# Optimization experiments

Hardware: AMD Instinct MI355X
Metric: run time of the kernel (lower is better)

Reference implementation:

```python
import jax, jax.numpy as jnp
import numpy as np

N = 80000      # num nodes total (8 graphs x 10000 vars)
E = 2560000    # num edges (avg degree 32)
EMB = 64       # embedding_layer_dim
POS = 16       # positional_features_dims
DG = 64        # dim_gnn
IN0 = 2 * EMB + POS          # 144, first conv in
IN1 = DG + 2 * EMB           # 192, second conv in / BN dim
EPS = 1e-5


def _lin_init(key, fan_in, fan_out):
    return jax.random.normal(key, (fan_in, fan_out), jnp.float32) / np.sqrt(fan_in)


def setup_inputs() -> dict:
    key = jax.random.key(0)
    ks = jax.random.split(key, 16)
    inp = {}
    inp["x1"] = jax.random.normal(ks[0], (N, EMB), jnp.float32)
    inp["x2"] = jax.random.normal(ks[1], (N, EMB), jnp.float32)
    inp["random_dims"] = jax.random.normal(ks[2], (N, POS), jnp.float32)
    inp["batch"] = jnp.sort(jax.random.randint(ks[3], (N,), 0, 8)).astype(jnp.int64)
    inp["x_j_mask"] = jnp.ones((E,), jnp.float32)
    inp["edge_index"] = jax.random.randint(ks[4], (2, E), 0, N).astype(jnp.int64)
    # GCNConv weights (PyG: lin then aggregate, bias added after)
    inp["conv0_w"] = _lin_init(ks[5], IN0, DG)
    inp["conv0_b"] = jnp.zeros((DG,), jnp.float32)
    inp["conv1_w"] = _lin_init(ks[6], IN1, DG)
    inp["conv1_b"] = jnp.zeros((DG,), jnp.float32)
    # BatchNorms after each conv (dim = DG + 2*EMB = 192)
    inp["bn0_g"] = jnp.ones((IN1,), jnp.float32)
    inp["bn0_b"] = jnp.zeros((IN1,), jnp.float32)
    inp["bn1_g"] = jnp.ones((IN1,), jnp.float32)
    inp["bn1_b"] = jnp.zeros((IN1,), jnp.float32)
    # MLP head: mlp[:-2] = [192->64, 64->64], mlp[-2] = 64->32 (final ->1 not applied here)
    inp["mlp0_w"] = _lin_init(ks[7], IN1, DG)
    inp["mlp0_b"] = jnp.zeros((DG,), jnp.float32)
    inp["mlp1_w"] = _lin_init(ks[8], DG, DG)
    inp["mlp1_b"] = jnp.zeros((DG,), jnp.float32)
    inp["mlp2_w"] = _lin_init(ks[9], DG, DG // 2)
    inp["mlp2_b"] = jnp.zeros((DG // 2,), jnp.float32)
    inp["bnm0_g"] = jnp.ones((DG,), jnp.float32)
    inp["bnm0_b"] = jnp.zeros((DG,), jnp.float32)
    inp["bnm1_g"] = jnp.ones((DG,), jnp.float32)
    inp["bnm1_b"] = jnp.zeros((DG,), jnp.float32)
    inp["bnm2_g"] = jnp.ones((DG // 2,), jnp.float32)
    inp["bnm2_b"] = jnp.zeros((DG // 2,), jnp.float32)
    return inp


def _batchnorm(x, g, b):
    m = x.mean(axis=0)
    v = jnp.var(x, axis=0)  # biased var, as torch BN uses for normalization
    return (x - m) * jax.lax.rsqrt(v + EPS) * g + b


def _gcn_conv(x, w, b, row, col, coef):
    # coef = deg^-1/2[row] * deg^-1/2[col] * x_j_mask, per edge
    h = x @ w                                   # [N, out]
    msg = coef[:, None] * h[row]                # gather + scale, [E, out]
    agg = jax.ops.segment_sum(msg, col, num_segments=N)
    return agg + b


def reference(x1, x2, random_dims, batch, x_j_mask, edge_index,
              conv0_w, conv0_b, conv1_w, conv1_b,
              bn0_g, bn0_b, bn1_g, bn1_b,
              mlp0_w, mlp0_b, mlp1_w, mlp1_b, mlp2_w, mlp2_b,
              bnm0_g, bnm0_b, bnm1_g, bnm1_b, bnm2_g, bnm2_b):
    row, col = edge_index[0], edge_index[1]
    # gcn_norm with add_self_loops=False, unit edge weights
    deg = jax.ops.segment_sum(jnp.ones((E,), x1.dtype), col, num_segments=N)
    dis = jnp.where(deg > 0, jax.lax.rsqrt(jnp.maximum(deg, 1.0)), 0.0)
    coef = dis[row] * dis[col] * x_j_mask       # edge mutilation mask applied to messages

    x = jnp.concatenate([x1, x2, random_dims], axis=1)  # [N, 144]
    # GNN layer 0
    h = jax.nn.elu(_gcn_conv(x, conv0_w, conv0_b, row, col, coef))
    x = _batchnorm(jnp.concatenate([x1, x2, h], axis=1), bn0_g, bn0_b)
    # GNN layer 1
    h = jax.nn.elu(_gcn_conv(x, conv1_w, conv1_b, row, col, coef))
    x = _batchnorm(jnp.concatenate([x1, x2, h], axis=1), bn1_g, bn1_b)
    # MLP head (from_node_to_out: mlp[:-2] with bns_mlp[:-1], then mlp[-2] with bns_mlp[-1])
    x = _batchnorm(jax.nn.elu(x @ mlp0_w + mlp0_b), bnm0_g, bnm0_b)
    x = _batchnorm(jax.nn.elu(x @ mlp1_w + mlp1_b), bnm1_g, bnm1_b)
    x = _batchnorm(jax.nn.elu(x @ mlp2_w + mlp2_b), bnm2_g, bnm2_b)
    return x  # [N, DG//2]
```

## Files before the change

kernel.cpp:

```cpp
#include <hip/hip_runtime.h>
#include <hip/hip_fp16.h>
#include <math.h>

#define NN 80000
#define NE 2560000
#define NBK 313
#define BCAP 10240
#define BN_EPS 1e-5f

typedef __attribute__((ext_vector_type(8))) short short8;
typedef __attribute__((ext_vector_type(8))) unsigned short ushort8;
typedef __attribute__((ext_vector_type(4))) float f32x4;

#define OFF_DIS     0
#define OFF_ROWPTR  80000
#define OFF_CURSOR  160004
#define OFF_DEG     240004
#define OFF_PERM    320004
#define OFF_XB      (OFF_PERM + 2*NE)
#define OFF_RDB     (OFF_XB + NN*64)
#define OFF_B1      (OFF_RDB + NN*16)
#define OFF_B2      (OFF_B1 + NN*32)
#define OFF_B3      (OFF_B2 + NN*32)
#define OFF_WP      (OFF_B3 + NN*32)
#define OFF_BV      (OFF_WP + 20480)
#define OFF_STATS   (OFF_BV + 320)

__device__ __forceinline__ ushort f2b(float f) {
    union { float f; unsigned u; } x; x.f = f;
    return (ushort)((x.u + 0x7FFF + ((x.u >> 16) & 1)) >> 16);
}
__device__ __forceinline__ float b2f(ushort u) {
    union { unsigned u; float f; } x; x.u = ((unsigned)u) << 16;
    return x.f;
}
__device__ __forceinline__ float h2f(unsigned bits15) {
    __half_raw hr; hr.x = (unsigned short)(bits15 & 0x7FFFu);
    return __half2float(*(__half*)&hr);
}

__global__ void __launch_bounds__(256) k_scat1(const int* __restrict__ erow,
                                               const int* __restrict__ ecol,
                                               const float* __restrict__ mask,
                                               int* __restrict__ bcursor,
                                               int2* __restrict__ pbuf) {
    __shared__ int hist[NBK], base[NBK];
    for (int i = threadIdx.x; i < NBK; i += 256) hist[i] = 0;
    __syncthreads();
    int e0 = blockIdx.x * 4096;
    int r[16], c[16], rk[16];
    float mk[16];
    #pragma unroll
    for (int i = 0; i < 16; i++) {
        int e = e0 + i * 256 + threadIdx.x;
        if (e < NE) {
            r[i] = erow[e]; c[i] = ecol[e]; mk[i] = mask[e];
            rk[i] = atomicAdd(&hist[c[i] >> 8], 1);
        } else c[i] = -1;
    }
    __syncthreads();
    for (int b = threadIdx.x; b < NBK; b += 256) {
        int h = hist[b];
        base[b] = h ? atomicAdd(&bcursor[b], h) : 0;
    }
    __syncthreads();
    #pragma unroll
    for (int i = 0; i < 16; i++) {
        if (c[i] >= 0) {
            int b = c[i] >> 8;
            int off = base[b] + rk[i];
            if (off < BCAP)
                pbuf[b * BCAP + off] = make_int2((r[i] << 8) | (c[i] & 255), __float_as_int(mk[i]));
        }
    }
}

__global__ void __launch_bounds__(256) k_cnt(const int* __restrict__ bcursor,
                                             const int2* __restrict__ pbuf,
                                             int* __restrict__ deg) {
    __shared__ int hist[256];
    int b = blockIdx.x, c0 = b << 8;
    int ncols = (NN - c0) < 256 ? (NN - c0) : 256;
    hist[threadIdx.x] = 0;
    __syncthreads();
    int cnt = bcursor[b];
    for (int i = threadIdx.x; i < cnt; i += 256)
        atomicAdd(&hist[pbuf[b * BCAP + i].x & 255], 1);
    __syncthreads();
    if (threadIdx.x < ncols) deg[c0 + threadIdx.x] = hist[threadIdx.x];
}

__global__ void __launch_bounds__(512) k_scanB(const int* __restrict__ bcursor,
                                               int* __restrict__ boff,
                                               int* __restrict__ rowptr) {
    __shared__ int s[512];
    int t = threadIdx.x;
    int v = t < NBK ? bcursor[t] : 0;
    s[t] = v;
    __syncthreads();
    for (int off = 1; off < 512; off <<= 1) {
        int u = t >= off ? s[t - off] : 0;
        __syncthreads();
        s[t] += u;
        __syncthreads();
    }
    if (t < NBK) boff[t] = s[t] - v;
    if (t == NBK - 1) rowptr[NN] = s[t];
}

__global__ void k_dis(const int* __restrict__ deg, float* __restrict__ dis) {
    int i = blockIdx.x * blockDim.x + threadIdx.x;
    if (i < NN) {
        int d = deg[i];
        dis[i] = d > 0 ? rsqrtf((float)d) : 0.f;
    }
}

__global__ void __launch_bounds__(256) k_place(const int* __restrict__ bcursor,
                                               const int* __restrict__ boff,
                                               const int* __restrict__ deg,
                                               const float* __restrict__ dis,
                                               const int2* __restrict__ pbuf,
                                               int* __restrict__ rowptr,
                                               unsigned* __restrict__ perm) {
    __shared__ int s[256], rbase[256], lcur[256];
    __shared__ float sdis[256];
    int b = blockIdx.x, c0 = b << 8;
    int ncols = (NN - c0) < 256 ? (NN - c0) : 256;
    int t = threadIdx.x;
    int d = t < ncols ? deg[c0 + t] : 0;
    s[t] = d;
    lcur[t] = 0;
    if (t < ncols) sdis[t] = dis[c0 + t];
    __syncthreads();
    for (int off = 1; off < 256; off <<= 1) {
        int u = t >= off ? s[t - off] : 0;
        __syncthreads();
        s[t] += u;
        __syncthreads();
    }
    rbase[t] = s[t] - d;
    __syncthreads();
    int gb = boff[b];
    if (t < ncols) rowptr[c0 + t] = gb + rbase[t];
    int cnt = bcursor[b];
    for (int i = t; i < cnt; i += 256) {
        int2 rec = pbuf[b * BCAP + i];
        int crel = rec.x & 255;
        unsigned row = (unsigned)(rec.x >> 8);
        float coef = dis[row] * sdis[crel] * __int_as_float(rec.y);
        __half hh = __float2half(coef);
        unsigned hb = (unsigned)__half_as_ushort(hh) & 0x7FFFu;
        int slot = gb + rbase[crel] + atomicAdd(&lcur[crel], 1);
        perm[slot] = (row << 15) | hb;
    }
}

__global__ void __launch_bounds__(256) k_prepstats(const float* __restrict__ x1,
                                                   const float* __restrict__ x2,
                                                   const float* __restrict__ rd,
                                                   ushort* __restrict__ xb,
                                                   ushort* __restrict__ rdb,
                                                   float* __restrict__ st) {
    int wave = threadIdx.x >> 6, lane = threadIdx.x & 63;
    float s1 = 0, q1 = 0, s2 = 0, q2 = 0;
    for (int n = blockIdx.x * 4 + wave; n < NN; n += gridDim.x * 4) {
        float a = x1[(size_t)n * 64 + lane];
        float b = x2[(size_t)n * 64 + lane];
        s1 += a; q1 += a * a; s2 += b; q2 += b * b;
        xb[(size_t)n * 128 + lane]      = f2b(a);
        xb[(size_t)n * 128 + 64 + lane] = f2b(b);
        if (lane < 32)
            rdb[(size_t)n * 32 + lane] = lane < 16 ? f2b(rd[(size_t)n * 16 + lane]) : 0;
    }
    __shared__ float red[4][256];
    red[0][threadIdx.x] = s1; red[1][threadIdx.x] = q1;
    red[2][threadIdx.x] = s2; red[3][threadIdx.x] = q2;
    __syncthreads();
    if (threadIdx.x < 64) {
        int l = threadIdx.x;
        atomicAdd(&st[l],       red[0][l] + red[0][l+64] + red[0][l+128] + red[0][l+192]);
        atomicAdd(&st[128 + l], red[1][l] + red[1][l+64] + red[1][l+128] + red[1][l+192]);
        atomicAdd(&st[64 + l],  red[2][l] + red[2][l+64] + red[2][l+128] + red[2][l+192]);
        atomicAdd(&st[192 + l], red[3][l] + red[3][l+64] + red[3][l+128] + red[3][l+192]);
    }
}

__global__ void k_foldw0(const float* __restrict__ W, ushort* __restrict__ Wp) {
    for (int idx = threadIdx.x; idx < 160 * 64; idx += 256) {
        int k = idx >> 6, c = idx & 63;
        float val = k < 144 ? W[k * 64 + c] : 0.f;
        int ks = k >> 5, j = k & 7, kg = (k >> 3) & 3;
        int l = kg * 16 + (c & 15), ct = c >> 4;
        Wp[((ks * 4 + ct) * 64 + l) * 8 + j] = f2b(val);
    }
}

__global__ void k_bnfold192(const float* __restrict__ xs,
                            const float* __restrict__ hsum, const float* __restrict__ hsq,
                            const float* __restrict__ g, const float* __restrict__ bnb,
                            const float* __restrict__ W,
                            const float* __restrict__ bias,
                            ushort* __restrict__ Wp, float* __restrict__ bvec) {
    __shared__ float scale[192], shift[192];
    int t = threadIdx.x;
    if (t < 192) {
        float s = t < 128 ? xs[t] : hsum[t - 128];
        float q = t < 128 ? xs[128 + t] : hsq[t - 128];
        float m = s * (1.f / NN);
        float var = q * (1.f / NN) - m * m;
        float sc = g[t] * rsqrtf(var + BN_EPS);
        scale[t] = sc;
        shift[t] = bnb[t] - m * sc;
    }
    __syncthreads();
    for (int idx = t; idx < 192 * 64; idx += 256) {
        int k = idx >> 6, c = idx & 63;
        float val = scale[k] * W[idx];
        int ks = k >> 5, j = k & 7, kg = (k >> 3) & 3;
        int l = kg * 16 + (c & 15), ct = c >> 4;
        Wp[((ks * 4 + ct) * 64 + l) * 8 + j] = f2b(val);
    }
    if (t < 64) {
        float acc = bias ? bias[t] : 0.f;
        for (int k = 0; k < 192; k++) acc += shift[k] * W[k * 64 + t];
        bvec[t] = acc;
    }
}

__global__ void k_bnfold64(const float* __restrict__ sum, const float* __restrict__ sq,
                           const float* __restrict__ g, const float* __restrict__ bnb,
                           const float* __restrict__ W, const float* __restrict__ bias,
                           ushort* __restrict__ Wp, float* __restrict__ bvec, int NCw) {
    __shared__ float scale[64], shift[64];
    int t = threadIdx.x;
    if (t < 64) {
        float m = sum[t] * (1.f / NN);
        float var = sq[t] * (1.f / NN) - m * m;
        float sc = g[t] * rsqrtf(var + BN_EPS);
        scale[t] = sc;
        shift[t] = bnb[t] - m * sc;
    }
    __syncthreads();
    int NCOLT = NCw >> 4;
    for (int idx = t; idx < 64 * NCw; idx += 256) {
        int k = idx / NCw, c = idx % NCw;
        float val = scale[k] * W[idx];
        int ks = k >> 5, j = k & 7, kg = (k >> 3) & 3;
        int l = kg * 16 + (c & 15), ct = c >> 4;
        Wp[((ks * NCOLT + ct) * 64 + l) * 8 + j] = f2b(val);
    }
    if (t < NCw) {
        float acc = bias[t];
        for (int k = 0; k < 64; k++) acc += shift[k] * W[k * NCw + t];
        bvec[t] = acc;
    }
}

template <int KSTEPS, int NCOLT, int KS1, int S1, int S2, bool EPI, bool OUTF32>
__global__ void __launch_bounds__(256) k_mfma(const ushort* __restrict__ A1,
                                              const ushort* __restrict__ A2,
                                              const ushort* __restrict__ Wp,
                                              const float* __restrict__ bvec,
                                              void* __restrict__ out,
                                              float* __restrict__ sum,
                                              float* __restrict__ sq) {
    const int NC = NCOLT * 16;
    __shared__ float cs[NC], cq[NC];
    int wave = threadIdx.x >> 6, lane = threadIdx.x & 63;
    int r0 = lane & 15, kg = lane >> 4;
    int rbase = blockIdx.x * 64 + wave * 16;
    if (EPI) {
        if (threadIdx.x < NC) { cs[threadIdx.x] = 0.f; cq[threadIdx.x] = 0.f; }
        __syncthreads();
    }
    f32x4 acc[NCOLT];
    #pragma unroll
    for (int ct = 0; ct < NCOLT; ct++) acc[ct] = (f32x4){0.f, 0.f, 0.f, 0.f};
    #pragma unroll
    for (int ks = 0; ks < KSTEPS; ks++) {
        const ushort* src = (ks < KS1)
            ? A1 + (size_t)(rbase + r0) * S1 + ks * 32 + kg * 8
            : A2 + (size_t)(rbase + r0) * S2 + (ks - KS1) * 32 + kg * 8;
        short8 a = *reinterpret_cast<const short8*>(src);
        #pragma unroll
        for (int ct = 0; ct < NCOLT; ct++) {
            short8 b = *reinterpret_cast<const short8*>(Wp + ((size_t)(ks * NCOLT + ct) * 64 + lane) * 8);
            acc[ct] = __builtin_amdgcn_mfma_f32_16x16x32_bf16(a, b, acc[ct], 0, 0, 0);
        }
    }
    float ss[NCOLT], qq[NCOLT];
    #pragma unroll
    for (int ct = 0; ct < NCOLT; ct++) {
        int c = ct * 16 + r0;
        float bv = bvec[c];
        ss[ct] = 0.f; qq[ct] = 0.f;
        #pragma unroll
        for (int r = 0; r < 4; r++) {
            int row = rbase + kg * 4 + r;
            float v = acc[ct][r] + bv;
            if (EPI) {
                v = v > 0.f ? v : (__expf(v) - 1.f);
                ss[ct] += v; qq[ct] += v * v;
            }
            if (OUTF32) ((float*)out)[(size_t)row * NC + c] = v;
            else        ((ushort*)out)[(size_t)row * NC + c] = f2b(v);
        }
    }
    if (EPI) {
        #pragma unroll
        for (int ct = 0; ct < NCOLT; ct++) {
            int c = ct * 16 + r0;
            atomicAdd(&cs[c], ss[ct]);
            atomicAdd(&cq[c], qq[ct]);
        }
        __syncthreads();
        if (threadIdx.x < NC) {
            atomicAdd(&sum[threadIdx.x], cs[threadIdx.x]);
            atomicAdd(&sq[threadIdx.x], cq[threadIdx.x]);
        }
    }
}

__global__ void __launch_bounds__(256) k_gather(const int* __restrict__ rowptr,
                                                const unsigned* __restrict__ perm,
                                                const ushort* __restrict__ h,
                                                const float* __restrict__ bias,
                                                ushort* __restrict__ out,
                                                float* __restrict__ sum,
                                                float* __restrict__ sq) {
    __shared__ float cs[64], cq[64];
    if (threadIdx.x < 64) { cs[threadIdx.x] = 0.f; cq[threadIdx.x] = 0.f; }
    __syncthreads();
    int wave = threadIdx.x >> 6, lane = threadIdx.x & 63;
    int g = lane >> 3, c8 = lane & 7;
    const ushort* hb = h + c8 * 8;
    float bs[8];
    #pragma unroll
    for (int j = 0; j < 8; j++) bs[j] = bias[c8 * 8 + j];
    float sArr[8], qArr[8];
    #pragma unroll
    for (int j = 0; j < 8; j++) { sArr[j] = 0.f; qArr[j] = 0.f; }

    for (int n = blockIdx.x * 4 + wave; n < NN; n += gridDim.x * 4) {
        int beg = rowptr[n], end = rowptr[n + 1];
        float acc[8];
        #pragma unroll
        for (int j = 0; j < 8; j++) acc[j] = 0.f;
        int e = beg;
        for (; e + 32 <= end; e += 32) {
            unsigned p0 = perm[e + g];
            unsigned p1 = perm[e + 8 + g];
            unsigned p2 = perm[e + 16 + g];
            unsigned p3 = perm[e + 24 + g];
            ushort8 h0 = *reinterpret_cast<const ushort8*>(hb + (size_t)(p0 >> 15) * 64);
            ushort8 h1 = *reinterpret_cast<const ushort8*>(hb + (size_t)(p1 >> 15) * 64);
            ushort8 h2 = *reinterpret_cast<const ushort8*>(hb + (size_t)(p2 >> 15) * 64);
            ushort8 h3 = *reinterpret_cast<const ushort8*>(hb + (size_t)(p3 >> 15) * 64);
            float c0 = h2f(p0), c1 = h2f(p1), c2 = h2f(p2), c3 = h2f(p3);
            #pragma unroll
            for (int j = 0; j < 8; j++) {
                acc[j] += c0 * b2f(h0[j]);
                acc[j] += c1 * b2f(h1[j]);
                acc[j] += c2 * b2f(h2[j]);
                acc[j] += c3 * b2f(h3[j]);
            }
        }
        for (; e < end; e += 8) {
            int ee = e + g;
            unsigned p = ee < end ? perm[ee] : 0u;
            ushort8 hv = *reinterpret_cast<const ushort8*>(hb + (size_t)(p >> 15) * 64);
            float cf = h2f(p);
            #pragma unroll
            for (int j = 0; j < 8; j++) acc[j] += cf * b2f(hv[j]);
        }
        #pragma unroll
        for (int j = 0; j < 8; j++) {
            float a = acc[j];
            a += __shfl_xor(a, 8, 64);
            a += __shfl_xor(a, 16, 64);
            a += __shfl_xor(a, 32, 64);
            acc[j] = a;
        }
        if (g == 0) {
            ushort8 ov;
            #pragma unroll
            for (int j = 0; j < 8; j++) {
                float v = acc[j] + bs[j];
                v = v > 0.f ? v : (__expf(v) - 1.f);
                sArr[j] += v; qArr[j] += v * v;
                ov[j] = f2b(v);
            }
            *reinterpret_cast<ushort8*>(out + (size_t)n * 64 + c8 * 8) = ov;
        }
    }
    if (g == 0) {
        #pragma unroll
        for (int j = 0; j < 8; j++) {
            atomicAdd(&cs[c8 * 8 + j], sArr[j]);
            atomicAdd(&cq[c8 * 8 + j], qArr[j]);
        }
    }
    __syncthreads();
    if (threadIdx.x < 64) {
        atomicAdd(&sum[threadIdx.x], cs[threadIdx.x]);
        atomicAdd(&sq[threadIdx.x], cq[threadIdx.x]);
    }
}

__global__ void k_out(const float* __restrict__ u2, const float* __restrict__ sum,
                      const float* __restrict__ sq, const float* __restrict__ g,
                      const float* __restrict__ bb, float* __restrict__ out) {
    int t = blockIdx.x * blockDim.x + threadIdx.x;
    if (t < NN * 32) {
        int c = t & 31;
        float m = sum[c] * (1.f / NN);
        float var = sq[c] * (1.f / NN) - m * m;
        float sc = g[c] * rsqrtf(var + BN_EPS);
        float sh = bb[c] - m * sc;
        out[t] = u2[t] * sc + sh;
    }
}

extern "C" void kernel_launch(void* const* d_in, const int* in_sizes, int n_in,
                              void* d_out, int out_size, void* d_ws, size_t ws_size,
                              hipStream_t stream) {
    const float* x1 = (const float*)d_in[0];
    const float* x2 = (const float*)d_in[1];
    const float* rd = (const float*)d_in[2];
    const float* mask = (const float*)d_in[4];
    const int* ei = (const int*)d_in[5];
    const int* erow = ei;
    const int* ecol = ei + NE;
    const float* conv0_w = (const float*)d_in[6];
    const float* conv0_b = (const float*)d_in[7];
    const float* conv1_w = (const float*)d_in[8];
    const float* conv1_b = (const float*)d_in[9];
    const float* bn0_g = (const float*)d_in[10];
    const float* bn0_b = (const float*)d_in[11];
    const float* bn1_g = (const float*)d_in[12];
    const float* bn1_b = (const float*)d_in[13];
    const float* mlp0_w = (const float*)d_in[14];
    const float* mlp0_b = (const float*)d_in[15];
    const float* mlp1_w = (const float*)d_in[16];
    const float* mlp1_b = (const float*)d_in[17];
    const float* mlp2_w = (const float*)d_in[18];
    const float* mlp2_b = (const float*)d_in[19];
    const float* bnm0_g = (const float*)d_in[20];
    const float* bnm0_b = (const float*)d_in[21];
    const float* bnm1_g = (const float*)d_in[22];
    const float* bnm1_b = (const float*)d_in[23];
    const float* bnm2_g = (const float*)d_in[24];
    const float* bnm2_b = (const float*)d_in[25];

    float* ws = (float*)d_ws;
    float* dis = ws + OFF_DIS;
    int* rowptr = (int*)(ws + OFF_ROWPTR);
    int* bcursor = (int*)(ws + OFF_CURSOR);
    int* boff = bcursor + 2048;
    int* deg = (int*)(ws + OFF_DEG);
    unsigned* perm = (unsigned*)(ws + OFF_PERM);
    ushort* xb = (ushort*)(ws + OFF_XB);
    ushort* rdb = (ushort*)(ws + OFF_RDB);
    ushort* B1 = (ushort*)(ws + OFF_B1);
    ushort* B2 = (ushort*)(ws + OFF_B2);
    ushort* B3 = (ushort*)(ws + OFF_B3);
    int2* pbuf = (int2*)(ws + OFF_B1);
    ushort* wp = (ushort*)(ws + OFF_WP);
    ushort* WP0 = wp, *WP1 = wp + 10240, *WP2 = wp + 22528, *WP3 = wp + 34816, *WP4 = wp + 38912;
    float* bv = ws + OFF_BV;
    float* st = ws + OFF_STATS;

    hipMemsetAsync(bcursor, 0, (size_t)1024 * 4, stream);
    hipMemsetAsync(bv, 0, (size_t)(320 + 1920) * 4, stream);

    k_scat1<<<(NE + 4095) / 4096, 256, 0, stream>>>(erow, ecol, mask, bcursor, pbuf);
    k_cnt<<<NBK, 256, 0, stream>>>(bcursor, pbuf, deg);
    k_scanB<<<1, 512, 0, stream>>>(bcursor, boff, rowptr);
    k_dis<<<NBK, 256, 0, stream>>>(deg, dis);
    k_place<<<NBK, 256, 0, stream>>>(bcursor, boff, deg, dis, pbuf, rowptr, perm);
    k_prepstats<<<1024, 256, 0, stream>>>(x1, x2, rd, xb, rdb, st);
    k_foldw0<<<1, 256, 0, stream>>>(conv0_w, WP0);

    const int GB = NN / 64;

    k_mfma<5, 4, 4, 128, 32, false, false><<<GB, 256, 0, stream>>>(xb, rdb, WP0, bv, B1, nullptr, nullptr);
    k_gather<<<2048, 256, 0, stream>>>(rowptr, perm, B1, conv0_b, B2, st + 256, st + 320);
    k_bnfold192<<<1, 256, 0, stream>>>(st, st + 256, st + 320, bn0_g, bn0_b, conv1_w, nullptr, WP1, bv + 64);

    k_mfma<6, 4, 4, 128, 64, false, false><<<GB, 256, 0, stream>>>(xb, B2, WP1, bv + 64, B1, nullptr, nullptr);
    k_gather<<<2048, 256, 0, stream>>>(rowptr, perm, B1, conv1_b, B3, st + 384, st + 448);
    k_bnfold192<<<1, 256, 0, stream>>>(st, st + 384, st + 448, bn1_g, bn1_b, mlp0_w, mlp0_b, WP2, bv + 128);

    k_mfma<6, 4, 4, 128, 64, true, false><<<GB, 256, 0, stream>>>(xb, B3, WP2, bv + 128, B2, st + 512, st + 576);
    k_bnfold64<<<1, 256, 0, stream>>>(st + 512, st + 576, bnm0_g, bnm0_b, mlp1_w, mlp1_b, WP3, bv + 192, 64);
    k_mfma<2, 4, 2, 64, 64, true, false><<<GB, 256, 0, stream>>>(B2, nullptr, WP3, bv + 192, B1, st + 640, st + 704);
    k_bnfold64<<<1, 256, 0, stream>>>(st + 640, st + 704, bnm1_g, bnm1_b, mlp2_w, mlp2_b, WP4, bv + 256, 32);
    k_mfma<2, 2, 2, 64, 64, true, true><<<GB, 256, 0, stream>>>(B1, nullptr, WP4, bv + 256, B3, st + 768, st + 800);
    k_out<<<(NN * 32 + 255) / 256, 256, 0, stream>>>((const float*)B3, st + 768, st + 800,
                                                     bnm2_g, bnm2_b, (float*)d_out);
}
```

Baseline: 606.4 us.

## Fuse CSR build kernels and fold source-degree scaling into GEMM epilogue

Merges the degree count, rsqrt-degree and placement kernels into one per-bucket build kernel, so there are fewer launches and no round trip through global deg. The source-side dis[row] factor moves out of edge-coefficient construction and into the conv GEMM epilogues, scaling each output row once. That removes a random dis gather per edge. The edge list is widened to int2 with an fp32 coefficient instead of packed row plus fp16, which doubles the bytes each gather reads per edge. The gather's main and tail loops are merged into one predicated loop.

```diff
diff --git a/kernel.cpp b/kernel.cpp
--- a/kernel.cpp
+++ b/kernel.cpp
@@ -34,10 +34,6 @@
     union { unsigned u; float f; } x; x.u = ((unsigned)u) << 16;
     return x.f;
 }
-__device__ __forceinline__ float h2f(unsigned bits15) {
-    __half_raw hr; hr.x = (unsigned short)(bits15 & 0x7FFFu);
-    return __half2float(*(__half*)&hr);
-}
 
 __global__ void __launch_bounds__(256) k_scat1(const int* __restrict__ erow,
                                                const int* __restrict__ ecol,
@@ -75,21 +71,6 @@
     }
 }
 
-__global__ void __launch_bounds__(256) k_cnt(const int* __restrict__ bcursor,
-                                             const int2* __restrict__ pbuf,
-                                             int* __restrict__ deg) {
-    __shared__ int hist[256];
-    int b = blockIdx.x, c0 = b << 8;
-    int ncols = (NN - c0) < 256 ? (NN - c0) : 256;
-    hist[threadIdx.x] = 0;
-    __syncthreads();
-    int cnt = bcursor[b];
-    for (int i = threadIdx.x; i < cnt; i += 256)
-        atomicAdd(&hist[pbuf[b * BCAP + i].x & 255], 1);
-    __syncthreads();
-    if (threadIdx.x < ncols) deg[c0 + threadIdx.x] = hist[threadIdx.x];
-}
-
 __global__ void __launch_bounds__(512) k_scanB(const int* __restrict__ bcursor,
                                                int* __restrict__ boff,
                                                int* __restrict__ rowptr) {
@@ -108,30 +89,29 @@
     if (t == NBK - 1) rowptr[NN] = s[t];
 }
 
-__global__ void k_dis(const int* __restrict__ deg, float* __restrict__ dis) {
-    int i = blockIdx.x * blockDim.x + threadIdx.x;
-    if (i < NN) {
-        int d = deg[i];
-        dis[i] = d > 0 ? rsqrtf((float)d) : 0.f;
-    }
-}
-
-__global__ void __launch_bounds__(256) k_place(const int* __restrict__ bcursor,
+__global__ void __launch_bounds__(256) k_build(const int* __restrict__ bcursor,
                                                const int* __restrict__ boff,
-                                               const int* __restrict__ deg,
-                                               const float* __restrict__ dis,
                                                const int2* __restrict__ pbuf,
+                                               float* __restrict__ dis,
                                                int* __restrict__ rowptr,
-                                               unsigned* __restrict__ perm) {
-    __shared__ int s[256], rbase[256], lcur[256];
+                                               int2* __restrict__ perm) {
+    __shared__ int hist[256], s[256], rbase[256], lcur[256];
     __shared__ float sdis[256];
     int b = blockIdx.x, c0 = b << 8;
     int ncols = (NN - c0) < 256 ? (NN - c0) : 256;
     int t = threadIdx.x;
-    int d = t < ncols ? deg[c0 + t] : 0;
+    hist[t] = 0;
+    lcur[t] = 0;
+    __syncthreads();
+    int cnt = bcursor[b];
+    for (int i = t; i < cnt; i += 256)
+        atomicAdd(&hist[pbuf[b * BCAP + i].x & 255], 1);
+    __syncthreads();
+    int d = (t < ncols) ? hist[t] : 0;
+    float dv = d > 0 ? rsqrtf((float)d) : 0.f;
+    sdis[t] = dv;
+    if (t < ncols) dis[c0 + t] = dv;
     s[t] = d;
-    lcur[t] = 0;
-    if (t < ncols) sdis[t] = dis[c0 + t];
     __syncthreads();
     for (int off = 1; off < 256; off <<= 1) {
         int u = t >= off ? s[t - off] : 0;
@@ -143,16 +123,13 @@
     __syncthreads();
     int gb = boff[b];
     if (t < ncols) rowptr[c0 + t] = gb + rbase[t];
-    int cnt = bcursor[b];
     for (int i = t; i < cnt; i += 256) {
         int2 rec = pbuf[b * BCAP + i];
         int crel = rec.x & 255;
-        unsigned row = (unsigned)(rec.x >> 8);
-        float coef = dis[row] * sdis[crel] * __int_as_float(rec.y);
-        __half hh = __float2half(coef);
-        unsigned hb = (unsigned)__half_as_ushort(hh) & 0x7FFFu;
+        int row = rec.x >> 8;
+        float coefS = sdis[crel] * __int_as_float(rec.y);
         int slot = gb + rbase[crel] + atomicAdd(&lcur[crel], 1);
-        perm[slot] = (row << 15) | hb;
+        perm[slot] = make_int2(row, __float_as_int(coefS));
     }
 }
 
@@ -257,11 +234,12 @@
     }
 }
 
-template <int KSTEPS, int NCOLT, int KS1, int S1, int S2, bool EPI, bool OUTF32>
+template <int KSTEPS, int NCOLT, int KS1, int S1, int S2, bool EPI, bool OUTF32, int DISW>
 __global__ void __launch_bounds__(256) k_mfma(const ushort* __restrict__ A1,
                                               const ushort* __restrict__ A2,
                                               const ushort* __restrict__ Wp,
                                               const float* __restrict__ bvec,
+                                              const float* __restrict__ disw,
                                               void* __restrict__ out,
                                               float* __restrict__ sum,
                                               float* __restrict__ sq) {
@@ -289,6 +267,11 @@
             acc[ct] = __builtin_amdgcn_mfma_f32_16x16x32_bf16(a, b, acc[ct], 0, 0, 0);
         }
     }
+    float dsv[4];
+    if (DISW) {
+        #pragma unroll
+        for (int r = 0; r < 4; r++) dsv[r] = disw[rbase + kg * 4 + r];
+    }
     float ss[NCOLT], qq[NCOLT];
     #pragma unroll
     for (int ct = 0; ct < NCOLT; ct++) {
@@ -299,6 +282,7 @@
         for (int r = 0; r < 4; r++) {
             int row = rbase + kg * 4 + r;
             float v = acc[ct][r] + bv;
+            if (DISW) v *= dsv[r];
             if (EPI) {
                 v = v > 0.f ? v : (__expf(v) - 1.f);
                 ss[ct] += v; qq[ct] += v * v;
@@ -323,7 +307,7 @@
 }
 
 __global__ void __launch_bounds__(256) k_gather(const int* __restrict__ rowptr,
-                                                const unsigned* __restrict__ perm,
+                                                const int2* __restrict__ perm,
                                                 const ushort* __restrict__ h,
                                                 const float* __restrict__ bias,
                                                 ushort* __restrict__ out,
@@ -347,17 +331,18 @@
         float acc[8];
         #pragma unroll
         for (int j = 0; j < 8; j++) acc[j] = 0.f;
-        int e = beg;
-        for (; e + 32 <= end; e += 32) {
-            unsigned p0 = perm[e + g];
-            unsigned p1 = perm[e + 8 + g];
-            unsigned p2 = perm[e + 16 + g];
-            unsigned p3 = perm[e + 24 + g];
-            ushort8 h0 = *reinterpret_cast<const ushort8*>(hb + (size_t)(p0 >> 15) * 64);
-            ushort8 h1 = *reinterpret_cast<const ushort8*>(hb + (size_t)(p1 >> 15) * 64);
-            ushort8 h2 = *reinterpret_cast<const ushort8*>(hb + (size_t)(p2 >> 15) * 64);
-            ushort8 h3 = *reinterpret_cast<const ushort8*>(hb + (size_t)(p3 >> 15) * 64);
-            float c0 = h2f(p0), c1 = h2f(p1), c2 = h2f(p2), c3 = h2f(p3);
+        for (int e = beg; e < end; e += 32) {
+            int e0 = e + g, e1 = e + 8 + g, e2 = e + 16 + g, e3 = e + 24 + g;
+            int2 p0 = e0 < end ? perm[e0] : make_int2(0, 0);
+            int2 p1 = e1 < end ? perm[e1] : make_int2(0, 0);
+            int2 p2 = e2 < end ? perm[e2] : make_int2(0, 0);
+            int2 p3 = e3 < end ? perm[e3] : make_int2(0, 0);
+            ushort8 h0 = *reinterpret_cast<const ushort8*>(hb + (size_t)p0.x * 64);
+            ushort8 h1 = *reinterpret_cast<const ushort8*>(hb + (size_t)p1.x * 64);
+            ushort8 h2 = *reinterpret_cast<const ushort8*>(hb + (size_t)p2.x * 64);
+            ushort8 h3 = *reinterpret_cast<const ushort8*>(hb + (size_t)p3.x * 64);
+            float c0 = __int_as_float(p0.y), c1 = __int_as_float(p1.y);
+            float c2 = __int_as_float(p2.y), c3 = __int_as_float(p3.y);
             #pragma unroll
             for (int j = 0; j < 8; j++) {
                 acc[j] += c0 * b2f(h0[j]);
@@ -365,14 +350,6 @@
                 acc[j] += c2 * b2f(h2[j]);
                 acc[j] += c3 * b2f(h3[j]);
             }
-        }
-        for (; e < end; e += 8) {
-            int ee = e + g;
-            unsigned p = ee < end ? perm[ee] : 0u;
-            ushort8 hv = *reinterpret_cast<const ushort8*>(hb + (size_t)(p >> 15) * 64);
-            float cf = h2f(p);
-            #pragma unroll
-            for (int j = 0; j < 8; j++) acc[j] += cf * b2f(hv[j]);
         }
         #pragma unroll
         for (int j = 0; j < 8; j++) {
@@ -458,8 +435,7 @@
     int* rowptr = (int*)(ws + OFF_ROWPTR);
     int* bcursor = (int*)(ws + OFF_CURSOR);
     int* boff = bcursor + 2048;
-    int* deg = (int*)(ws + OFF_DEG);
-    unsigned* perm = (unsigned*)(ws + OFF_PERM);
+    int2* perm = (int2*)(ws + OFF_PERM);
     ushort* xb = (ushort*)(ws + OFF_XB);
     ushort* rdb = (ushort*)(ws + OFF_RDB);
     ushort* B1 = (ushort*)(ws + OFF_B1);
@@ -475,28 +451,26 @@
     hipMemsetAsync(bv, 0, (size_t)(320 + 1920) * 4, stream);
 
     k_scat1<<<(NE + 4095) / 4096, 256, 0, stream>>>(erow, ecol, mask, bcursor, pbuf);
-    k_cnt<<<NBK, 256, 0, stream>>>(bcursor, pbuf, deg);
     k_scanB<<<1, 512, 0, stream>>>(bcursor, boff, rowptr);
-    k_dis<<<NBK, 256, 0, stream>>>(deg, dis);
-    k_place<<<NBK, 256, 0, stream>>>(bcursor, boff, deg, dis, pbuf, rowptr, perm);
+    k_build<<<NBK, 256, 0, stream>>>(bcursor, boff, pbuf, dis, rowptr, perm);
     k_prepstats<<<1024, 256, 0, stream>>>(x1, x2, rd, xb, rdb, st);
     k_foldw0<<<1, 256, 0, stream>>>(conv0_w, WP0);
 
     const int GB = NN / 64;
 
-    k_mfma<5, 4, 4, 128, 32, false, false><<<GB, 256, 0, stream>>>(xb, rdb, WP0, bv, B1, nullptr, nullptr);
+    k_mfma<5, 4, 4, 128, 32, false, false, 1><<<GB, 256, 0, stream>>>(xb, rdb, WP0, bv, dis, B1, nullptr, nullptr);
     k_gather<<<2048, 256, 0, stream>>>(rowptr, perm, B1, conv0_b, B2, st + 256, st + 320);
     k_bnfold192<<<1, 256, 0, stream>>>(st, st + 256, st + 320, bn0_g, bn0_b, conv1_w, nullptr, WP1, bv + 64);
 
-    k_mfma<6, 4, 4, 128, 64, false, false><<<GB, 256, 0, stream>>>(xb, B2, WP1, bv + 64, B1, nullptr, nullptr);
+    k_mfma<6, 4, 4, 128, 64, false, false, 1><<<GB, 256, 0, stream>>>(xb, B2, WP1, bv + 64, dis, B1, nullptr, nullptr);
     k_gather<<<2048, 256, 0, stream>>>(rowptr, perm, B1, conv1_b, B3, st + 384, st + 448);
     k_bnfold192<<<1, 256, 0, stream>>>(st, st + 384, st + 448, bn1_g, bn1_b, mlp0_w, mlp0_b, WP2, bv + 128);
 
-    k_mfma<6, 4, 4, 128, 64, true, false><<<GB, 256, 0, stream>>>(xb, B3, WP2, bv + 128, B2, st + 512, st + 576);
+    k_mfma<6, 4, 4, 128, 64, true, false, 0><<<GB, 256, 0, stream>>>(xb, B3, WP2, bv + 128, nullptr, B2, st + 512, st + 576);
     k_bnfold64<<<1, 256, 0, stream>>>(st + 512, st + 576, bnm0_g, bnm0_b, mlp1_w, mlp1_b, WP3, bv + 192, 64);
-    k_mfma<2, 4, 2, 64, 64, true, false><<<GB, 256, 0, stream>>>(B2, nullptr, WP3, bv + 192, B1, st + 640, st + 704);
+    k_mfma<2, 4, 2, 64, 64, true, false, 0><<<GB, 256, 0, stream>>>(B2, nullptr, WP3, bv + 192, nullptr, B1, st + 640, st + 704);
     k_bnfold64<<<1, 256, 0, stream>>>(st + 640, st + 704, bnm1_g, bnm1_b, mlp2_w, mlp2_b, WP4, bv + 256, 32);
-    k_mfma<2, 2, 2, 64, 64, true, true><<<GB, 256, 0, stream>>>(B1, nullptr, WP4, bv + 256, B3, st + 768, st + 800);
+    k_mfma<2, 2, 2, 64, 64, true, true, 0><<<GB, 256, 0, stream>>>(B1, nullptr, WP4, bv + 256, nullptr, B3, st + 768, st + 800);
     k_out<<<(NN * 32 + 255) / 256, 256, 0, stream>>>((const float*)B3, st + 768, st + 800,
                                                      bnm2_g, bnm2_b, (float*)d_out);
 }
```

Result: faster. 585.4 us (-3.5%).
